# Kernel tuning notes

Hardware: AMD Instinct MI355X
Metric: run time of the kernel (lower is better)

The kernel has to match this reference:

```python
import jax, jax.numpy as jnp
import numpy as np

R_MAX = 5.0
NUM_BASIS = 8
CUTOFF_P = 6
N_LAYERS = 3
C = 64          # hidden_mul / channels of irreps_conv_out (64x0e+64x1o)
Z = 4           # element_number
AVG_DEG = 32.0  # num-neighbor normalization (E/N)
SQRT3 = 1.7320508075688772
SQRT2 = 1.4142135623730951


def _radial_embedding(r):
    # Bessel basis * polynomial cutoff (RadialEdgeEmbedding)
    rs = jnp.maximum(r, 1e-9)
    n = jnp.arange(1, NUM_BASIS + 1, dtype=r.dtype)  # (B,)
    bessel = jnp.sqrt(2.0 / R_MAX) * jnp.sin(n * jnp.pi * rs[:, None] / R_MAX) / rs[:, None]
    x = r / R_MAX
    p = float(CUTOFF_P)
    fc = (1.0
          - (p + 1.0) * (p + 2.0) / 2.0 * x ** CUTOFF_P
          + p * (p + 2.0) * x ** (CUTOFF_P + 1)
          - p * (p + 1.0) / 2.0 * x ** (CUTOFF_P + 2))
    fc = jnp.where(x < 1.0, fc, 0.0)
    return bessel * fc[:, None]  # (E, NUM_BASIS)


def setup_inputs() -> dict:
    key = jax.random.key(0)
    ks = jax.random.split(key, 20)
    N, E, B = 16000, 512000, 16
    atom_type = jax.random.randint(ks[0], (N,), 0, Z)
    # atoms in a 4A box so most edge lengths fall inside r_max=5
    atom_pos = jax.random.uniform(ks[1], (N, 3), dtype=jnp.float32) * 4.0
    edge_src = jax.random.randint(ks[2], (E,), 0, N)
    edge_dst = jax.random.randint(ks[3], (E,), 0, N)
    edge_cell_shift = jnp.zeros((E, 3), jnp.float32)
    cell = jnp.tile(jnp.eye(3, dtype=jnp.float32) * 10.0, (B, 1, 1)) \
        + 0.01 * jax.random.normal(ks[4], (B, 3, 3), jnp.float32)
    image_index = jax.random.randint(ks[5], (N,), 0, B)
    g = lambda k, s, fan: jax.random.normal(k, s, jnp.float32) / np.sqrt(fan)
    return {
        'atom_type': atom_type, 'atom_pos': atom_pos,
        'edge_src': edge_src, 'edge_dst': edge_dst,
        'edge_cell_shift': edge_cell_shift, 'cell': cell, 'image_index': image_index,
        'w_lin_in': g(ks[6], (Z, C), Z),
        'mlp_w1': g(ks[7], (N_LAYERS, NUM_BASIS, 64), NUM_BASIS),
        'mlp_b1': jnp.zeros((N_LAYERS, 64), jnp.float32),
        'mlp_w2': g(ks[8], (N_LAYERS, 64, 5 * C), 64),
        'w_self_s': g(ks[9], (N_LAYERS, C, C), C),
        'w_self_v': g(ks[10], (N_LAYERS, C, C), C),
        'w_gate': g(ks[11], (N_LAYERS, C, C), C),
        'w_lin1': g(ks[12], (C, 16), C),
        'w_lin2': g(ks[13], (16, 1), 16),
    }


def reference(atom_type, atom_pos, edge_src, edge_dst, edge_cell_shift, cell,
              image_index, w_lin_in, mlp_w1, mlp_b1, mlp_w2,
              w_self_s, w_self_v, w_gate, w_lin1, w_lin2):
    N = atom_pos.shape[0]
    # edge vectors with periodic cell shift
    edge_vec = atom_pos[edge_dst] - atom_pos[edge_src]
    edge_vec = edge_vec + jnp.einsum('ni,nij->nj', edge_cell_shift,
                                     cell.reshape(-1, 3, 3)[image_index[edge_src]])
    r = jnp.linalg.norm(edge_vec, axis=1)                      # (E,)
    unit = edge_vec / jnp.maximum(r, 1e-9)[:, None]
    # spherical harmonics lmax=1, component normalization: y0=1 (implicit), y1=sqrt(3)*unit
    y1 = SQRT3 * unit                                           # (E, 3)
    emb = _radial_embedding(r)                                  # (E, NUM_BASIS)

    # one-hot embedding + input linear (one-hot is all 0e -> scalar channels only)
    onehot = jax.nn.one_hot(atom_type, Z, dtype=atom_pos.dtype)
    s = onehot @ w_lin_in                                       # (N, C) l=0 features
    v = jnp.zeros((N, C, 3), atom_pos.dtype)                    # (N, C, 3) l=1 features

    inv_sqrt_deg = 1.0 / np.sqrt(AVG_DEG)
    for L in range(N_LAYERS):
        # radial MLP -> per-edge per-channel tensor-product path weights
        w = jax.nn.silu(emb @ mlp_w1[L] + mlp_b1[L]) @ mlp_w2[L]  # (E, 5C)
        w1, w2, w3, w4, w5 = jnp.split(w, 5, axis=1)              # (E, C) each
        s_src = s[edge_src]                                       # (E, C)
        v_src = v[edge_src]                                       # (E, C, 3)
        vdoty = jnp.einsum('ecx,ex->ec', v_src, y1)
        # CG tensor-product paths (l<=1):
        m_s = w1 * s_src + w2 * vdoty / SQRT3                     # 0x0->0, 1x1->0
        m_v = (w3[:, :, None] * s_src[:, :, None] * y1[:, None, :]      # 0x1->1
               + w4[:, :, None] * v_src                                  # 1x0->1
               + w5[:, :, None] * jnp.cross(v_src, y1[:, None, :]) / SQRT2)  # 1x1->1
        agg_s = jax.ops.segment_sum(m_s, edge_dst, num_segments=N) * inv_sqrt_deg
        agg_v = jax.ops.segment_sum(m_v, edge_dst, num_segments=N) * inv_sqrt_deg
        # gated self-interaction + resnet
        gate = jax.nn.sigmoid(agg_s @ w_gate[L])                  # (N, C)
        s = s + jax.nn.silu(agg_s @ w_self_s[L])
        v = v + jnp.einsum('ncx,cd->ndx', agg_v, w_self_v[L]) * gate[:, :, None]

    # o3.Linear to 16x0e then 1x0e (only scalar channels map to 0e outputs)
    atomic_energy = (s @ w_lin1) @ w_lin2                         # (N, 1)
    atomic_energy = atomic_energy * 1.0                           # atomic_scale
    return atomic_energy
```

## Files before the change

kernel.cpp:

```cpp
#include <hip/hip_runtime.h>
#include <hip/hip_fp16.h>
#include <math.h>

#define NUM_BASIS 8
#define SQRT3 1.7320508075688772f
#define SQRT2 1.4142135623730951f
#define INV_SQRT_DEG 0.17677669529663687f
#define PI_F 3.14159265358979323846f

typedef _Float16 half8 __attribute__((ext_vector_type(8)));
typedef float float4v __attribute__((ext_vector_type(4)));

__device__ __forceinline__ float sigmoidf_(float x) { return 1.0f / (1.0f + __expf(-x)); }
__device__ __forceinline__ float siluf_(float x) { return x * sigmoidf_(x); }

__device__ __forceinline__ void unp2(unsigned u, float& a, float& b) {
    __half2 h = *reinterpret_cast<__half2*>(&u);
    float2 f = __half22float2(h);
    a = f.x; b = f.y;
}
__device__ __forceinline__ unsigned pk2(float a, float b) {
    __half2 h = __floats2half2_rn(a, b);
    return *reinterpret_cast<unsigned*>(&h);
}

__global__ __launch_bounds__(256) void count_deg(
    const int* __restrict__ dst, int* __restrict__ deg, int E)
{
    int base = (blockIdx.x * blockDim.x + threadIdx.x) * 4;
    if (base + 3 < E) {
        int4 d4 = *(const int4*)(dst + base);
        atomicAdd(&deg[d4.x], 1);
        atomicAdd(&deg[d4.y], 1);
        atomicAdd(&deg[d4.z], 1);
        atomicAdd(&deg[d4.w], 1);
    } else {
        for (int e = base; e < E; e++) atomicAdd(&deg[dst[e]], 1);
    }
}

__global__ __launch_bounds__(1024) void scan_deg(
    const int* __restrict__ deg, int* __restrict__ cursor, int N)
{
    __shared__ int wsum[16];
    __shared__ int carry_s, tot_s;
    int tid = threadIdx.x;
    int wid = tid >> 6, lane = tid & 63;
    if (tid == 0) carry_s = 0;
    __syncthreads();
    for (int base = 0; base < N; base += 16384) {
        int i0 = base + tid * 16;
        int v[16];
        int sum = 0;
        #pragma unroll
        for (int k = 0; k < 16; k++) {
            int i = i0 + k;
            v[k] = (i < N) ? deg[i] : 0;
            sum += v[k];
        }
        int incl = sum;
        #pragma unroll
        for (int off = 1; off < 64; off <<= 1) {
            int t = __shfl_up(incl, off);
            if (lane >= off) incl += t;
        }
        if (lane == 63) wsum[wid] = incl;
        __syncthreads();
        if (wid == 0 && lane < 16) {
            int wv = wsum[lane];
            int wincl = wv;
            #pragma unroll
            for (int off = 1; off < 16; off <<= 1) {
                int t = __shfl_up(wincl, off);
                if (lane >= off) wincl += t;
            }
            wsum[lane] = wincl - wv;
            if (lane == 15) tot_s = wincl;
        }
        __syncthreads();
        int carry = carry_s;
        int run = carry + wsum[wid] + incl - sum;
        #pragma unroll
        for (int k = 0; k < 16; k++) {
            int i = i0 + k;
            if (i < N) cursor[i] = run;
            run += v[k];
        }
        __syncthreads();
        if (tid == 0) carry_s = carry + tot_s;
        __syncthreads();
    }
}

__global__ __launch_bounds__(256) void edge_pre_scatter(
    const float* __restrict__ pos, const int* __restrict__ src,
    const int* __restrict__ dst, const float* __restrict__ cs,
    const float* __restrict__ cell, const int* __restrict__ img,
    int* __restrict__ cursor, _Float16* __restrict__ emb,
    uint2* __restrict__ y14, int2* __restrict__ sdp, int E)
{
    int e = blockIdx.x * blockDim.x + threadIdx.x;
    if (e >= E) return;
    int si = src[e], di = dst[e];
    int slot = atomicAdd(&cursor[di], 1);
    sdp[slot] = make_int2(si, di);
    float vx = pos[di*3+0] - pos[si*3+0];
    float vy = pos[di*3+1] - pos[si*3+1];
    float vz = pos[di*3+2] - pos[si*3+2];
    float c0 = cs[(size_t)e*3+0], c1 = cs[(size_t)e*3+1], c2 = cs[(size_t)e*3+2];
    const float* M = cell + (size_t)img[si] * 9;
    vx += c0*M[0] + c1*M[3] + c2*M[6];
    vy += c0*M[1] + c1*M[4] + c2*M[7];
    vz += c0*M[2] + c1*M[5] + c2*M[8];
    float r  = sqrtf(vx*vx + vy*vy + vz*vz);
    float rs = fmaxf(r, 1e-9f);
    float inv = 1.0f / rs;
    uint2 yv;
    yv.x = pk2(SQRT3*vx*inv, SQRT3*vy*inv);
    yv.y = pk2(SQRT3*vz*inv, 0.f);
    y14[slot] = yv;
    float x = r * (1.0f / 5.0f);
    float x2 = x*x, x6 = x2*x2*x2;
    float fc = 1.0f - 28.0f*x6 + 48.0f*x6*x - 21.0f*x6*x2;
    if (x >= 1.0f) fc = 0.0f;
    float pre = sqrtf(2.0f / 5.0f) * inv * fc;
    float t = PI_F * rs * (1.0f / 5.0f);
    half8 ev;
    #pragma unroll
    for (int n = 1; n <= NUM_BASIS; n++)
        ev[n-1] = (_Float16)(pre * __sinf((float)n * t));
    *(half8*)(emb + (size_t)slot*NUM_BASIS) = ev;
}

__global__ __launch_bounds__(256) void prep_weights(
    const float* __restrict__ W2, _Float16* __restrict__ w2f,
    const float* __restrict__ Wg, const float* __restrict__ Ws,
    const float* __restrict__ Wv, _Float16* __restrict__ wgtf,
    const float* __restrict__ Wl1, const float* __restrict__ Wl2,
    float* __restrict__ wl12)
{
    int idx = blockIdx.x * blockDim.x + threadIdx.x;
    if (idx < 64) {
        float a = 0.f;
        #pragma unroll
        for (int j = 0; j < 16; j++) a = fmaf(Wl1[idx*16 + j], Wl2[j], a);
        wl12[idx] = a;
    }
    if (idx < 3 * 20480) {
        int L  = idx / 20480;
        int r  = idx % 20480;
        int cg = r / 5120;
        int r2 = r % 5120;
        int p  = r2 / 1024;
        int r3 = r2 % 1024;
        int kh = r3 / 512;
        int r4 = r3 % 512;
        int lane = r4 / 8;
        int j  = r4 % 8;
        int k = kh*32 + (lane >> 4)*8 + j;
        int n = p*64 + cg*16 + (lane & 15);
        float val = W2[(size_t)L*20480 + k*320 + n];
        if (p == 1)      val *= 0.5773502691896258f;
        else if (p == 4) val *= 0.7071067811865476f;
        w2f[idx] = (_Float16)val;
    } else if (idx < 3*20480 + 3*3*4096) {
        int idx2 = idx - 3*20480;
        int L   = idx2 / 12288;
        int rem = idx2 % 12288;
        int mat = rem / 4096;
        int r2  = rem % 4096;
        int cg  = r2 / 1024;
        int r3  = r2 % 1024;
        int kh  = r3 / 512;
        int r4  = r3 % 512;
        int lane = r4 / 8;
        int j   = r4 % 8;
        int k = kh*32 + (lane >> 4)*8 + j;
        int n = cg*16 + (lane & 15);
        const float* src = (mat == 0) ? Wg : (mat == 1) ? Ws : Wv;
        wgtf[idx2] = (_Float16)src[(size_t)L*4096 + k*64 + n];
    }
}

__device__ __forceinline__ void mlp1_afrag(
    const _Float16* __restrict__ emb, const float* __restrict__ W1,
    const float* __restrict__ B1, int eA, int q, half8 afrag[2])
{
    half8 ev = *(const half8*)(emb + (size_t)eA*8);
    float em[8];
    #pragma unroll
    for (int j = 0; j < 8; j++) em[j] = (float)ev[j];
    #pragma unroll
    for (int kh = 0; kh < 2; kh++) {
        int kb = kh*32 + q*8;
        float hv[8];
        float4 b0 = *(const float4*)(B1 + kb);
        float4 b1 = *(const float4*)(B1 + kb + 4);
        hv[0]=b0.x; hv[1]=b0.y; hv[2]=b0.z; hv[3]=b0.w;
        hv[4]=b1.x; hv[5]=b1.y; hv[6]=b1.z; hv[7]=b1.w;
        #pragma unroll
        for (int jj = 0; jj < 8; jj++) {
            float4 wa = *(const float4*)(W1 + jj*64 + kb);
            float4 wb = *(const float4*)(W1 + jj*64 + kb + 4);
            hv[0] = fmaf(em[jj], wa.x, hv[0]);
            hv[1] = fmaf(em[jj], wa.y, hv[1]);
            hv[2] = fmaf(em[jj], wa.z, hv[2]);
            hv[3] = fmaf(em[jj], wa.w, hv[3]);
            hv[4] = fmaf(em[jj], wb.x, hv[4]);
            hv[5] = fmaf(em[jj], wb.y, hv[5]);
            hv[6] = fmaf(em[jj], wb.z, hv[6]);
            hv[7] = fmaf(em[jj], wb.w, hv[7]);
        }
        #pragma unroll
        for (int j = 0; j < 8; j++)
            afrag[kh][j] = (_Float16)siluf_(hv[j]);
    }
}

__global__ __launch_bounds__(256) void edge_msg_mfma_l0(
    const _Float16* __restrict__ emb, const uint2* __restrict__ y14,
    const int2* __restrict__ sdp,
    const int* __restrict__ type, const float* __restrict__ wlin,
    const float* __restrict__ W1, const float* __restrict__ B1,
    const _Float16* __restrict__ w2f,
    float* __restrict__ aggs, float* __restrict__ aggx,
    float* __restrict__ aggy, float* __restrict__ aggz, int E)
{
    __shared__ _Float16 w2s[8192];
    {
        half8* dstv = (half8*)w2s;
        const half8* srcv = (const half8*)w2f;
        #pragma unroll
        for (int k = 0; k < 4; k++) {
            int t  = threadIdx.x + k*256;
            int cg = t >> 8;
            int r  = t & 255;
            int pp = r >> 7;
            int rk = r & 127;
            dstv[t] = srcv[cg*640 + pp*256 + rk];
        }
    }
    __syncthreads();

    int wave  = (blockIdx.x * blockDim.x + threadIdx.x) >> 6;
    int lane  = threadIdx.x & 63;
    int wbase = wave * 16;
    if (wbase >= E) return;
    int q   = lane >> 4;
    int col = lane & 15;

    int eb = wbase + q*4;
    int d[4], tt[4];
    float y1x[4], y1y[4], y1z[4];
    #pragma unroll
    for (int r = 0; r < 4; r++) {
        int2 sv = sdp[eb + r];
        tt[r] = type[sv.x];
        d[r]  = sv.y;
        uint2 yv = y14[eb + r];
        float dummy;
        unp2(yv.x, y1x[r], y1y[r]);
        unp2(yv.y, y1z[r], dummy);
    }

    half8 afrag[2];
    mlp1_afrag(emb, W1, B1, wbase + col, q, afrag);

    int dnq = __shfl_down(d[0], 16);
    int nd3 = (q == 3) ? -1 : dnq;
    int df = d[0], dl = d[3];
    bool U = (df == dl);
    int dlp = __shfl_up(dl, 16);
    bool link = (q > 0) && (dlp == df);

    #pragma unroll
    for (int cg = 0; cg < 4; cg++) {
        float4v a1 = {0,0,0,0}, a3 = {0,0,0,0};
        const _Float16* wbp = w2s + ((size_t)cg*2048) + (size_t)lane*8;
        {
            half8 b10 = *(const half8*)(wbp + 0*512);
            half8 b11 = *(const half8*)(wbp + 1*512);
            half8 b30 = *(const half8*)(wbp + 2*512);
            half8 b31 = *(const half8*)(wbp + 3*512);
            a1 = __builtin_amdgcn_mfma_f32_16x16x32_f16(afrag[0], b10, a1, 0, 0, 0);
            a1 = __builtin_amdgcn_mfma_f32_16x16x32_f16(afrag[1], b11, a1, 0, 0, 0);
            a3 = __builtin_amdgcn_mfma_f32_16x16x32_f16(afrag[0], b30, a3, 0, 0, 0);
            a3 = __builtin_amdgcn_mfma_f32_16x16x32_f16(afrag[1], b31, a3, 0, 0, 0);
        }
        int c = cg*16 + col;

        float ms[4], mx[4], my[4], mz[4];
        #pragma unroll
        for (int r = 0; r < 4; r++) {
            float s = wlin[tt[r]*64 + c];
            float w3s = a3[r] * s;
            ms[r] = a1[r] * s;
            mx[r] = w3s * y1x[r];
            my[r] = w3s * y1y[r];
            mz[r] = w3s * y1z[r];
        }
        #pragma unroll
        for (int r = 1; r < 4; r++) {
            if (d[r] == d[r-1]) {
                ms[r] += ms[r-1]; mx[r] += mx[r-1];
                my[r] += my[r-1]; mz[r] += mz[r-1];
            }
        }
        float Cs = 0.f, Cx = 0.f, Cy = 0.f, Cz = 0.f;
        #pragma unroll
        for (int it = 0; it < 3; it++) {
            float es = ms[3] + (U ? Cs : 0.f);
            float ex = mx[3] + (U ? Cx : 0.f);
            float ey = my[3] + (U ? Cy : 0.f);
            float ez = mz[3] + (U ? Cz : 0.f);
            float ts = __shfl_up(es, 16);
            float tx = __shfl_up(ex, 16);
            float ty = __shfl_up(ey, 16);
            float tz = __shfl_up(ez, 16);
            Cs = link ? ts : 0.f; Cx = link ? tx : 0.f;
            Cy = link ? ty : 0.f; Cz = link ? tz : 0.f;
        }
        bool hr = true;
        #pragma unroll
        for (int r = 0; r < 4; r++) {
            if (r > 0) hr = hr && (d[r] == d[r-1]);
            float fs = ms[r] + (hr ? Cs : 0.f);
            float fx = mx[r] + (hr ? Cx : 0.f);
            float fy = my[r] + (hr ? Cy : 0.f);
            float fz = mz[r] + (hr ? Cz : 0.f);
            int ndx = (r < 3) ? d[r+1] : nd3;
            if (ndx != d[r] && d[r] >= 0) {
                size_t ai = (size_t)d[r]*64 + c;
                atomicAdd(aggs + ai, fs);
                atomicAdd(aggx + ai, fx);
                atomicAdd(aggy + ai, fy);
                atomicAdd(aggz + ai, fz);
            }
        }
    }
}

__device__ __forceinline__ void process_half(
    const _Float16* __restrict__ w2s, const half8 afrag[2],
    const uint2 pf[4][2], const int d[4], int nd3, bool U, bool link,
    bool live, const float* y1x, const float* y1y, const float* y1z,
    int cgh, int col,
    float* __restrict__ aggs, float* __restrict__ aggx,
    float* __restrict__ aggy, float* __restrict__ aggz)
{
    int lane = threadIdx.x & 63;
    #pragma unroll
    for (int cgl = 0; cgl < 2; cgl++) {
        float4v acc[5];
        #pragma unroll
        for (int p = 0; p < 5; p++) acc[p] = (float4v){0.f, 0.f, 0.f, 0.f};
        const _Float16* wbp = w2s + ((size_t)cgl*5120) + (size_t)lane*8;
        #pragma unroll
        for (int p = 0; p < 5; p++) {
            half8 bf0 = *(const half8*)(wbp + ((size_t)(p*2 + 0))*512);
            half8 bf1 = *(const half8*)(wbp + ((size_t)(p*2 + 1))*512);
            acc[p] = __builtin_amdgcn_mfma_f32_16x16x32_f16(afrag[0], bf0, acc[p], 0, 0, 0);
            acc[p] = __builtin_amdgcn_mfma_f32_16x16x32_f16(afrag[1], bf1, acc[p], 0, 0, 0);
        }
        int c = (cgh*2 + cgl)*16 + col;

        float ms[4], mx[4], my[4], mz[4];
        #pragma unroll
        for (int r = 0; r < 4; r++) {
            float fsx, fvx, fvy, fvz;
            unp2(pf[r][cgl].x, fsx, fvx);
            unp2(pf[r][cgl].y, fvy, fvz);
            float yx = y1x[r], yy = y1y[r], yz = y1z[r];
            float w1 = acc[0][r], w2 = acc[1][r], w3 = acc[2][r];
            float w4 = acc[3][r], w5 = acc[4][r];
            float vdoty = fvx*yx + fvy*yy + fvz*yz;
            ms[r] = fmaf(w1, fsx, w2*vdoty);
            float w3s = w3*fsx;
            float cx = fvy*yz - fvz*yy;
            float cy = fvz*yx - fvx*yz;
            float cz = fvx*yy - fvy*yx;
            mx[r] = fmaf(w3s, yx, fmaf(w4, fvx, w5*cx));
            my[r] = fmaf(w3s, yy, fmaf(w4, fvy, w5*cy));
            mz[r] = fmaf(w3s, yz, fmaf(w4, fvz, w5*cz));
        }
        #pragma unroll
        for (int r = 1; r < 4; r++) {
            if (d[r] == d[r-1]) {
                ms[r] += ms[r-1]; mx[r] += mx[r-1];
                my[r] += my[r-1]; mz[r] += mz[r-1];
            }
        }
        float Cs = 0.f, Cx = 0.f, Cy = 0.f, Cz = 0.f;
        #pragma unroll
        for (int it = 0; it < 3; it++) {
            float es = ms[3] + (U ? Cs : 0.f);
            float ex = mx[3] + (U ? Cx : 0.f);
            float ey = my[3] + (U ? Cy : 0.f);
            float ez = mz[3] + (U ? Cz : 0.f);
            float ts = __shfl_up(es, 16);
            float tx = __shfl_up(ex, 16);
            float ty = __shfl_up(ey, 16);
            float tz = __shfl_up(ez, 16);
            Cs = link ? ts : 0.f; Cx = link ? tx : 0.f;
            Cy = link ? ty : 0.f; Cz = link ? tz : 0.f;
        }
        bool hr = true;
        #pragma unroll
        for (int r = 0; r < 4; r++) {
            if (r > 0) hr = hr && (d[r] == d[r-1]);
            float fs = ms[r] + (hr ? Cs : 0.f);
            float fx = mx[r] + (hr ? Cx : 0.f);
            float fy = my[r] + (hr ? Cy : 0.f);
            float fz = mz[r] + (hr ? Cz : 0.f);
            int ndx = (r < 3) ? d[r+1] : nd3;
            if (ndx != d[r] && d[r] >= 0 && live) {
                size_t ai = (size_t)d[r]*64 + c;
                atomicAdd(aggs + ai, fs);
                atomicAdd(aggx + ai, fx);
                atomicAdd(aggy + ai, fy);
                atomicAdd(aggz + ai, fz);
            }
        }
    }
}

__global__ __launch_bounds__(256) void edge_msg_mfma(
    const _Float16* __restrict__ emb, const uint2* __restrict__ y14,
    const int2* __restrict__ sdp,
    const uint2* __restrict__ nf,
    const float* __restrict__ W1, const float* __restrict__ B1,
    const _Float16* __restrict__ w2f,
    float* __restrict__ aggs, float* __restrict__ aggx,
    float* __restrict__ aggy, float* __restrict__ aggz, int E)
{
    __shared__ _Float16 w2s[10240];
    {
        half8* dstv = (half8*)w2s;
        const half8* srcv = (const half8*)w2f;
        #pragma unroll
        for (int k = 0; k < 5; k++)
            dstv[threadIdx.x + k*256] = srcv[threadIdx.x + k*256];
    }
    __syncthreads();

    int wave  = (blockIdx.x * blockDim.x + threadIdx.x) >> 6;
    int lane  = threadIdx.x & 63;
    int wbase = wave * 16;
    bool live = wbase < E;
    int wb2   = live ? wbase : 0;
    int q   = lane >> 4;
    int col = lane & 15;

    int eb = wb2 + q*4;
    int d[4], si[4];
    float y1x[4], y1y[4], y1z[4];
    #pragma unroll
    for (int r = 0; r < 4; r++) {
        int2 sv = sdp[eb + r];
        si[r] = sv.x;
        d[r]  = sv.y;
        uint2 yv = y14[eb + r];
        float dummy;
        unp2(yv.x, y1x[r], y1y[r]);
        unp2(yv.y, y1z[r], dummy);
    }

    uint2 pf[4][2];
    #pragma unroll
    for (int r = 0; r < 4; r++) {
        size_t nb = (size_t)si[r] * 64 + col;
        pf[r][0] = nf[nb];
        pf[r][1] = nf[nb + 16];
    }

    half8 afrag[2];
    mlp1_afrag(emb, W1, B1, wb2 + col, q, afrag);

    int dnq = __shfl_down(d[0], 16);
    int nd3 = (q == 3) ? -1 : dnq;
    int df = d[0], dl = d[3];
    bool U = (df == dl);
    int dlp = __shfl_up(dl, 16);
    bool link = (q > 0) && (dlp == df);

    process_half(w2s, afrag, pf, d, nd3, U, link, live,
                 y1x, y1y, y1z, 0, col, aggs, aggx, aggy, aggz);

    #pragma unroll
    for (int r = 0; r < 4; r++) {
        size_t nb = (size_t)si[r] * 64 + 32 + col;
        pf[r][0] = nf[nb];
        pf[r][1] = nf[nb + 16];
    }

    asm volatile("s_waitcnt lgkmcnt(0)" ::: "memory");
    __builtin_amdgcn_s_barrier();
    asm volatile("" ::: "memory");

    {
        half8* dstv = (half8*)w2s;
        const half8* srcv = (const half8*)w2f + 1280;
        #pragma unroll
        for (int k = 0; k < 5; k++)
            dstv[threadIdx.x + k*256] = srcv[threadIdx.x + k*256];
    }

    asm volatile("s_waitcnt lgkmcnt(0)" ::: "memory");
    __builtin_amdgcn_s_barrier();
    asm volatile("" ::: "memory");

    process_half(w2s, afrag, pf, d, nd3, U, link, live,
                 y1x, y1y, y1z, 1, col, aggs, aggx, aggy, aggz);
}

__global__ __launch_bounds__(256) void node_update_mfma(
    uint2* __restrict__ nf,
    float* __restrict__ aggs, float* __restrict__ aggx,
    float* __restrict__ aggy, float* __restrict__ aggz,
    const _Float16* __restrict__ wgtf,
    const int* __restrict__ type, const float* __restrict__ wlin,
    const float* __restrict__ wl12,
    float* __restrict__ out, int first, int do_out, int N)
{
    __shared__ _Float16 wgs[12288];
    {
        half8* dstv = (half8*)wgs;
        const half8* srcv = (const half8*)wgtf;
        #pragma unroll
        for (int k = 0; k < 6; k++)
            dstv[threadIdx.x + k*256] = srcv[threadIdx.x + k*256];
    }

    int wave  = (blockIdx.x * blockDim.x + threadIdx.x) >> 6;
    int lane  = threadIdx.x & 63;
    int wbase = wave * 16;
    bool active = wbase < N;
    int q = lane >> 4, col = lane & 15;

    int nodeA = active ? (wbase + col) : 0;
    if (nodeA >= N) nodeA = N - 1;
    size_t nb = (size_t)nodeA * 64 + q * 8;
    half8 af0[2], af1[2], af2[2], af3[2];
    #pragma unroll
    for (int kh = 0; kh < 2; kh++) {
        const float* p0 = aggs + nb + kh*32;
        const float* p1 = aggx + nb + kh*32;
        const float* p2 = aggy + nb + kh*32;
        const float* p3 = aggz + nb + kh*32;
        float4 a0 = *(const float4*)p0, b0 = *(const float4*)(p0+4);
        float4 a1 = *(const float4*)p1, b1 = *(const float4*)(p1+4);
        float4 a2 = *(const float4*)p2, b2 = *(const float4*)(p2+4);
        float4 a3 = *(const float4*)p3, b3 = *(const float4*)(p3+4);
        af0[kh][0]=(_Float16)(a0.x*INV_SQRT_DEG); af0[kh][1]=(_Float16)(a0.y*INV_SQRT_DEG);
        af0[kh][2]=(_Float16)(a0.z*INV_SQRT_DEG); af0[kh][3]=(_Float16)(a0.w*INV_SQRT_DEG);
        af0[kh][4]=(_Float16)(b0.x*INV_SQRT_DEG); af0[kh][5]=(_Float16)(b0.y*INV_SQRT_DEG);
        af0[kh][6]=(_Float16)(b0.z*INV_SQRT_DEG); af0[kh][7]=(_Float16)(b0.w*INV_SQRT_DEG);
        af1[kh][0]=(_Float16)(a1.x*INV_SQRT_DEG); af1[kh][1]=(_Float16)(a1.y*INV_SQRT_DEG);
        af1[kh][2]=(_Float16)(a1.z*INV_SQRT_DEG); af1[kh][3]=(_Float16)(a1.w*INV_SQRT_DEG);
        af1[kh][4]=(_Float16)(b1.x*INV_SQRT_DEG); af1[kh][5]=(_Float16)(b1.y*INV_SQRT_DEG);
        af1[kh][6]=(_Float16)(b1.z*INV_SQRT_DEG); af1[kh][7]=(_Float16)(b1.w*INV_SQRT_DEG);
        af2[kh][0]=(_Float16)(a2.x*INV_SQRT_DEG); af2[kh][1]=(_Float16)(a2.y*INV_SQRT_DEG);
        af2[kh][2]=(_Float16)(a2.z*INV_SQRT_DEG); af2[kh][3]=(_Float16)(a2.w*INV_SQRT_DEG);
        af2[kh][4]=(_Float16)(b2.x*INV_SQRT_DEG); af2[kh][5]=(_Float16)(b2.y*INV_SQRT_DEG);
        af2[kh][6]=(_Float16)(b2.z*INV_SQRT_DEG); af2[kh][7]=(_Float16)(b2.w*INV_SQRT_DEG);
        af3[kh][0]=(_Float16)(a3.x*INV_SQRT_DEG); af3[kh][1]=(_Float16)(a3.y*INV_SQRT_DEG);
        af3[kh][2]=(_Float16)(a3.z*INV_SQRT_DEG); af3[kh][3]=(_Float16)(a3.w*INV_SQRT_DEG);
        af3[kh][4]=(_Float16)(b3.x*INV_SQRT_DEG); af3[kh][5]=(_Float16)(b3.y*INV_SQRT_DEG);
        af3[kh][6]=(_Float16)(b3.z*INV_SQRT_DEG); af3[kh][7]=(_Float16)(b3.w*INV_SQRT_DEG);
    }

    int tt[4];
    #pragma unroll
    for (int r = 0; r < 4; r++) {
        int nd = wbase + q*4 + r;
        tt[r] = type[(active && nd < N) ? nd : 0];
    }

    __syncthreads();

    float epart[4] = {0.f, 0.f, 0.f, 0.f};

    #pragma unroll
    for (int cg = 0; cg < 4; cg++) {
        const _Float16* bp = wgs + (size_t)lane * 8;
        half8 bg0 = *(const half8*)(bp + ((size_t)((0*4 + cg)*2 + 0))*512);
        half8 bg1 = *(const half8*)(bp + ((size_t)((0*4 + cg)*2 + 1))*512);
        half8 bs0 = *(const half8*)(bp + ((size_t)((1*4 + cg)*2 + 0))*512);
        half8 bs1 = *(const half8*)(bp + ((size_t)((1*4 + cg)*2 + 1))*512);
        half8 bv0 = *(const half8*)(bp + ((size_t)((2*4 + cg)*2 + 0))*512);
        half8 bv1 = *(const half8*)(bp + ((size_t)((2*4 + cg)*2 + 1))*512);
        float4v ag = {0,0,0,0}, as = {0,0,0,0};
        float4v ox = {0,0,0,0}, oy = {0,0,0,0}, oz = {0,0,0,0};
        ag = __builtin_amdgcn_mfma_f32_16x16x32_f16(af0[0], bg0, ag, 0, 0, 0);
        ag = __builtin_amdgcn_mfma_f32_16x16x32_f16(af0[1], bg1, ag, 0, 0, 0);
        as = __builtin_amdgcn_mfma_f32_16x16x32_f16(af0[0], bs0, as, 0, 0, 0);
        as = __builtin_amdgcn_mfma_f32_16x16x32_f16(af0[1], bs1, as, 0, 0, 0);
        ox = __builtin_amdgcn_mfma_f32_16x16x32_f16(af1[0], bv0, ox, 0, 0, 0);
        ox = __builtin_amdgcn_mfma_f32_16x16x32_f16(af1[1], bv1, ox, 0, 0, 0);
        oy = __builtin_amdgcn_mfma_f32_16x16x32_f16(af2[0], bv0, oy, 0, 0, 0);
        oy = __builtin_amdgcn_mfma_f32_16x16x32_f16(af2[1], bv1, oy, 0, 0, 0);
        oz = __builtin_amdgcn_mfma_f32_16x16x32_f16(af3[0], bv0, oz, 0, 0, 0);
        oz = __builtin_amdgcn_mfma_f32_16x16x32_f16(af3[1], bv1, oz, 0, 0, 0);

        if (!active) continue;
        int c = cg*16 + col;
        float wlc = wl12[c];
        #pragma unroll
        for (int r = 0; r < 4; r++) {
            int nd = wbase + q*4 + r;
            bool wr = nd < N;
            size_t ni = (size_t)nd*64 + c;
            float sx, vx, vy, vz;
            if (first) {
                sx = wlin[tt[r]*64 + c];
                vx = 0.f; vy = 0.f; vz = 0.f;
            } else {
                uint2 cur = nf[wr ? ni : 0];
                unp2(cur.x, sx, vx);
                unp2(cur.y, vy, vz);
            }
            float gate = sigmoidf_(ag[r]);
            sx += siluf_(as[r]);
            vx += ox[r] * gate;
            vy += oy[r] * gate;
            vz += oz[r] * gate;
            if (wr) {
                uint2 nv;
                nv.x = pk2(sx, vx);
                nv.y = pk2(vy, vz);
                nf[ni] = nv;
                aggs[ni] = 0.f;
                aggx[ni] = 0.f;
                aggy[ni] = 0.f;
                aggz[ni] = 0.f;
                epart[r] = fmaf(sx, wlc, epart[r]);
            }
        }
    }
    if (do_out && active) {
        #pragma unroll
        for (int r = 0; r < 4; r++) {
            float e = epart[r];
            e += __shfl_xor(e, 1);
            e += __shfl_xor(e, 2);
            e += __shfl_xor(e, 4);
            e += __shfl_xor(e, 8);
            int nd = wbase + q*4 + r;
            if (col == 0 && nd < N) out[nd] = e;
        }
    }
}

extern "C" void kernel_launch(void* const* d_in, const int* in_sizes, int n_in,
                              void* d_out, int out_size, void* d_ws, size_t ws_size,
                              hipStream_t stream)
{
    const int*   atom_type = (const int*)  d_in[0];
    const float* pos       = (const float*)d_in[1];
    const int*   src       = (const int*)  d_in[2];
    const int*   dst       = (const int*)  d_in[3];
    const float* cs        = (const float*)d_in[4];
    const float* cell      = (const float*)d_in[5];
    const int*   img       = (const int*)  d_in[6];
    const float* wlin_in   = (const float*)d_in[7];
    const float* mw1       = (const float*)d_in[8];
    const float* mb1       = (const float*)d_in[9];
    const float* mw2       = (const float*)d_in[10];
    const float* wss       = (const float*)d_in[11];
    const float* wsv       = (const float*)d_in[12];
    const float* wg        = (const float*)d_in[13];
    const float* wl1       = (const float*)d_in[14];
    const float* wl2       = (const float*)d_in[15];
    int N = in_sizes[0];
    int E = in_sizes[2];

    char* w = (char*)d_ws;
    _Float16* emb = (_Float16*)w; w += (size_t)E * 8 * sizeof(_Float16);
    uint2*  y14  = (uint2*)w;  w += (size_t)E * sizeof(uint2);
    int2*   sdp  = (int2*)w;   w += (size_t)E * sizeof(int2);
    uint2*  nf   = (uint2*)w;  w += (size_t)N * 64 * sizeof(uint2);
    float*  agg  = (float*)w;  w += (size_t)N * 64 * 4 * sizeof(float);
    _Float16* w2f  = (_Float16*)w; w += (size_t)3 * 20480 * sizeof(_Float16);
    _Float16* wgtf = (_Float16*)w; w += (size_t)3 * 3 * 4096 * sizeof(_Float16);
    float*  wl12 = (float*)w;  w += 64 * sizeof(float);
    int*    deg  = (int*)w;    w += (size_t)N * sizeof(int);
    int*    curs = (int*)w;    w += (size_t)N * sizeof(int);

    size_t NC = (size_t)N * 64;
    float* aggs = agg;
    float* aggx = agg + NC;
    float* aggy = agg + 2*NC;
    float* aggz = agg + 3*NC;

    hipMemsetAsync(deg, 0, (size_t)N * sizeof(int), stream);
    hipMemsetAsync(agg, 0, NC * 4 * sizeof(float), stream);
    count_deg<<<(E/4 + 255) / 256, 256, 0, stream>>>(dst, deg, E);
    scan_deg<<<1, 1024, 0, stream>>>(deg, curs, N);
    int prep_n = 3*20480 + 3*3*4096;
    prep_weights<<<(prep_n + 255) / 256, 256, 0, stream>>>(
        mw2, w2f, wg, wss, wsv, wgtf, wl1, wl2, wl12);
    edge_pre_scatter<<<(E + 255) / 256, 256, 0, stream>>>(
        pos, src, dst, cs, cell, img, curs, emb, y14, sdp, E);

    int eblocks = (E + 63) / 64;
    int nblocks = (N + 63) / 64;

    edge_msg_mfma_l0<<<eblocks, 256, 0, stream>>>(
        emb, y14, sdp, atom_type, wlin_in,
        mw1, mb1, w2f, aggs, aggx, aggy, aggz, E);
    node_update_mfma<<<nblocks, 256, 0, stream>>>(
        nf, aggs, aggx, aggy, aggz, wgtf, atom_type, wlin_in, wl12,
        (float*)d_out, 1, 0, N);

    for (int L = 1; L < 3; L++) {
        edge_msg_mfma<<<eblocks, 256, 0, stream>>>(
            emb, y14, sdp, nf,
            mw1 + L * 8 * 64, mb1 + L * 64, w2f + (size_t)L * 20480,
            aggs, aggx, aggy, aggz, E);
        node_update_mfma<<<nblocks, 256, 0, stream>>>(
            nf, aggs, aggx, aggy, aggz,
            wgtf + (size_t)L * 12288, atom_type, wlin_in, wl12,
            (float*)d_out, 0, (L == 2) ? 1 : 0, N);
    }
}
```

Before: 461.0 us.

## Precompute radial MLP hidden layer into workspace buffers before edge kernels

Adds a separate kernel that evaluates the first radial MLP layer (8→64 with SiLU) per edge and writes the fp16 activations to a workspace buffer. The edge message kernels are templated to load these precomputed A-fragments instead of recomputing the dense layer inline. When the workspace allows, all three layers are precomputed up front. This trades redundant in-kernel FMAs for extra global memory traffic, about 64 MB per layer of fp16 writes and reads, which may cost more than it saves on a bandwidth-bound edge pass. Whether it runs depends on workspace size.

```diff
diff --git a/kernel.cpp b/kernel.cpp
--- a/kernel.cpp
+++ b/kernel.cpp
@@ -182,6 +182,42 @@
     }
 }
 
+__global__ __launch_bounds__(256) void mlp1_pre(
+    const _Float16* __restrict__ emb, const float* __restrict__ W1,
+    const float* __restrict__ B1, _Float16* __restrict__ hA, int E)
+{
+    int idx = blockIdx.x * blockDim.x + threadIdx.x;
+    int e = idx >> 3;
+    if (e >= E) return;
+    int kb = (idx & 7) * 8;
+    half8 ev = *(const half8*)(emb + (size_t)e*8);
+    float em[8];
+    #pragma unroll
+    for (int j = 0; j < 8; j++) em[j] = (float)ev[j];
+    float hv[8];
+    float4 b0 = *(const float4*)(B1 + kb);
+    float4 b1 = *(const float4*)(B1 + kb + 4);
+    hv[0]=b0.x; hv[1]=b0.y; hv[2]=b0.z; hv[3]=b0.w;
+    hv[4]=b1.x; hv[5]=b1.y; hv[6]=b1.z; hv[7]=b1.w;
+    #pragma unroll
+    for (int jj = 0; jj < 8; jj++) {
+        float4 wa = *(const float4*)(W1 + jj*64 + kb);
+        float4 wb = *(const float4*)(W1 + jj*64 + kb + 4);
+        hv[0] = fmaf(em[jj], wa.x, hv[0]);
+        hv[1] = fmaf(em[jj], wa.y, hv[1]);
+        hv[2] = fmaf(em[jj], wa.z, hv[2]);
+        hv[3] = fmaf(em[jj], wa.w, hv[3]);
+        hv[4] = fmaf(em[jj], wb.x, hv[4]);
+        hv[5] = fmaf(em[jj], wb.y, hv[5]);
+        hv[6] = fmaf(em[jj], wb.z, hv[6]);
+        hv[7] = fmaf(em[jj], wb.w, hv[7]);
+    }
+    half8 out;
+    #pragma unroll
+    for (int j = 0; j < 8; j++) out[j] = (_Float16)siluf_(hv[j]);
+    *(half8*)(hA + (size_t)e*64 + kb) = out;
+}
+
 __device__ __forceinline__ void mlp1_afrag(
     const _Float16* __restrict__ emb, const float* __restrict__ W1,
     const float* __restrict__ B1, int eA, int q, half8 afrag[2])
@@ -217,9 +253,10 @@
     }
 }
 
+template<bool PRE>
 __global__ __launch_bounds__(256) void edge_msg_mfma_l0(
-    const _Float16* __restrict__ emb, const uint2* __restrict__ y14,
-    const int2* __restrict__ sdp,
+    const _Float16* __restrict__ emb, const _Float16* __restrict__ hA,
+    const uint2* __restrict__ y14, const int2* __restrict__ sdp,
     const int* __restrict__ type, const float* __restrict__ wlin,
     const float* __restrict__ W1, const float* __restrict__ B1,
     const _Float16* __restrict__ w2f,
@@ -248,6 +285,13 @@
     if (wbase >= E) return;
     int q   = lane >> 4;
     int col = lane & 15;
+
+    half8 afrag[2];
+    if (PRE) {
+        const _Float16* hp = hA + (size_t)(wbase + col)*64 + q*8;
+        afrag[0] = *(const half8*)(hp);
+        afrag[1] = *(const half8*)(hp + 32);
+    }
 
     int eb = wbase + q*4;
     int d[4], tt[4];
@@ -263,8 +307,7 @@
         unp2(yv.y, y1z[r], dummy);
     }
 
-    half8 afrag[2];
-    mlp1_afrag(emb, W1, B1, wbase + col, q, afrag);
+    if (!PRE) mlp1_afrag(emb, W1, B1, wbase + col, q, afrag);
 
     int dnq = __shfl_down(d[0], 16);
     int nd3 = (q == 3) ? -1 : dnq;
@@ -424,9 +467,10 @@
     }
 }
 
+template<bool PRE>
 __global__ __launch_bounds__(256) void edge_msg_mfma(
-    const _Float16* __restrict__ emb, const uint2* __restrict__ y14,
-    const int2* __restrict__ sdp,
+    const _Float16* __restrict__ emb, const _Float16* __restrict__ hA,
+    const uint2* __restrict__ y14, const int2* __restrict__ sdp,
     const uint2* __restrict__ nf,
     const float* __restrict__ W1, const float* __restrict__ B1,
     const _Float16* __restrict__ w2f,
@@ -450,6 +494,13 @@
     int wb2   = live ? wbase : 0;
     int q   = lane >> 4;
     int col = lane & 15;
+
+    half8 afrag[2];
+    if (PRE) {
+        const _Float16* hp = hA + (size_t)(wb2 + col)*64 + q*8;
+        afrag[0] = *(const half8*)(hp);
+        afrag[1] = *(const half8*)(hp + 32);
+    }
 
     int eb = wb2 + q*4;
     int d[4], si[4];
@@ -473,8 +524,7 @@
         pf[r][1] = nf[nb + 16];
     }
 
-    half8 afrag[2];
-    mlp1_afrag(emb, W1, B1, wb2 + col, q, afrag);
+    if (!PRE) mlp1_afrag(emb, W1, B1, wb2 + col, q, afrag);
 
     int dnq = __shfl_down(d[0], 16);
     int nd3 = (q == 3) ? -1 : dnq;
@@ -686,6 +736,13 @@
     int*    deg  = (int*)w;    w += (size_t)N * sizeof(int);
     int*    curs = (int*)w;    w += (size_t)N * sizeof(int);
 
+    size_t used   = (size_t)(w - (char*)d_ws);
+    size_t hbytes = (size_t)E * 64 * sizeof(_Float16);
+    int nh = 0;
+    if      (ws_size >= used + 3*hbytes) nh = 3;
+    else if (ws_size >= used + hbytes)   nh = 1;
+    _Float16* hbuf = (_Float16*)w;
+
     size_t NC = (size_t)N * 64;
     float* aggs = agg;
     float* aggx = agg + NC;
@@ -704,19 +761,46 @@
 
     int eblocks = (E + 63) / 64;
     int nblocks = (N + 63) / 64;
-
-    edge_msg_mfma_l0<<<eblocks, 256, 0, stream>>>(
-        emb, y14, sdp, atom_type, wlin_in,
-        mw1, mb1, w2f, aggs, aggx, aggy, aggz, E);
+    int hblocks = (E * 8 + 255) / 256;
+
+    if (nh == 3) {
+        for (int L = 0; L < 3; L++)
+            mlp1_pre<<<hblocks, 256, 0, stream>>>(
+                emb, mw1 + L * 8 * 64, mb1 + L * 64, hbuf + (size_t)L * E * 64, E);
+    }
+
+    if (nh >= 1) {
+        _Float16* h0 = hbuf;
+        if (nh == 1)
+            mlp1_pre<<<hblocks, 256, 0, stream>>>(emb, mw1, mb1, h0, E);
+        edge_msg_mfma_l0<true><<<eblocks, 256, 0, stream>>>(
+            emb, h0, y14, sdp, atom_type, wlin_in,
+            mw1, mb1, w2f, aggs, aggx, aggy, aggz, E);
+    } else {
+        edge_msg_mfma_l0<false><<<eblocks, 256, 0, stream>>>(
+            emb, nullptr, y14, sdp, atom_type, wlin_in,
+            mw1, mb1, w2f, aggs, aggx, aggy, aggz, E);
+    }
     node_update_mfma<<<nblocks, 256, 0, stream>>>(
         nf, aggs, aggx, aggy, aggz, wgtf, atom_type, wlin_in, wl12,
         (float*)d_out, 1, 0, N);
 
     for (int L = 1; L < 3; L++) {
-        edge_msg_mfma<<<eblocks, 256, 0, stream>>>(
-            emb, y14, sdp, nf,
-            mw1 + L * 8 * 64, mb1 + L * 64, w2f + (size_t)L * 20480,
-            aggs, aggx, aggy, aggz, E);
+        if (nh >= 1) {
+            _Float16* hL = (nh == 3) ? hbuf + (size_t)L * E * 64 : hbuf;
+            if (nh == 1)
+                mlp1_pre<<<hblocks, 256, 0, stream>>>(
+                    emb, mw1 + L * 8 * 64, mb1 + L * 64, hL, E);
+            edge_msg_mfma<true><<<eblocks, 256, 0, stream>>>(
+                emb, hL, y14, sdp, nf,
+                mw1 + L * 8 * 64, mb1 + L * 64, w2f + (size_t)L * 20480,
+                aggs, aggx, aggy, aggz, E);
+        } else {
+            edge_msg_mfma<false><<<eblocks, 256, 0, stream>>>(
+                emb, nullptr, y14, sdp, nf,
+                mw1 + L * 8 * 64, mb1 + L * 64, w2f + (size_t)L * 20480,
+                aggs, aggx, aggy, aggz, E);
+        }
         node_update_mfma<<<nblocks, 256, 0, stream>>>(
             nf, aggs, aggx, aggy, aggz,
             wgtf + (size_t)L * 12288, atom_type, wlin_in, wl12,
```

Result: slower. 522.6 us (+13.4%).
